# Performance work log

Measured on AMD Instinct MI355X. Metric: run time of the kernel, lower is better.

The kernel has to match this reference:

```python
import jax, jax.numpy as jnp
import numpy as np

N_NODES = 50000
N_EDGES = 800000
GNN_IN, GNN_HID, COMB = 256, 64, 64
MLP_IN, MLP_HID = 256, 512


def glorot(key, shape):
    fan_in, fan_out = shape[0], shape[1]
    s = jnp.sqrt(6.0 / (fan_in + fan_out)).astype(jnp.float32)
    return jax.random.uniform(key, shape, jnp.float32, -s, s)


def setup_inputs() -> dict:
    key = jax.random.key(0)
    ks = jax.random.split(key, 12)
    x = jax.random.normal(ks[0], (N_NODES, GNN_IN), jnp.float32)
    edge_index = jax.random.randint(ks[1], (2, N_EDGES), 0, N_NODES, jnp.int64 if jax.config.jax_enable_x64 else jnp.int32)
    edge_attr = jax.random.uniform(ks[2], (N_EDGES,), jnp.float32)
    user_features = jax.random.normal(ks[3], (N_NODES, MLP_IN), jnp.float32)
    params = {
        'gcn1_W': glorot(ks[4], (GNN_IN, GNN_HID)),
        'gcn1_b': jnp.zeros((GNN_HID,), jnp.float32),
        'gcn2_W': glorot(ks[5], (GNN_HID, COMB)),
        'gcn2_b': jnp.zeros((COMB,), jnp.float32),
        'fc1_W': glorot(ks[6], (MLP_IN, MLP_HID)),
        'fc1_b': jnp.zeros((MLP_HID,), jnp.float32),
        'fc2_W': glorot(ks[7], (MLP_HID, COMB)),
        'fc2_b': jnp.zeros((COMB,), jnp.float32),
        'fcf_W': glorot(ks[8], (2 * COMB, 1)),
        'fcf_b': jnp.zeros((1,), jnp.float32),
    }
    return dict(x=x, edge_index=edge_index, edge_attr=edge_attr,
                user_features=user_features, **params)


def gcn_conv(x, W, b, src, dst, ew, n_nodes):
    # PyG GCNConv: transform, add self-loops (weight 1), sym-normalize, scatter-add.
    h = x @ W  # [N, out]
    loop = jnp.arange(n_nodes, dtype=src.dtype)
    src_sl = jnp.concatenate([src, loop])
    dst_sl = jnp.concatenate([dst, loop])
    ew_sl = jnp.concatenate([ew, jnp.ones((n_nodes,), ew.dtype)])
    deg = jax.ops.segment_sum(ew_sl, dst_sl, num_segments=n_nodes)
    dinv = jnp.where(deg > 0, jax.lax.rsqrt(jnp.maximum(deg, 1e-12)), 0.0)
    norm = dinv[src_sl] * ew_sl * dinv[dst_sl]  # [E+N]
    msg = h[src_sl] * norm[:, None]             # gather + scale
    out = jax.ops.segment_sum(msg, dst_sl, num_segments=n_nodes)
    return out + b


def reference(x, edge_index, edge_attr, user_features,
              gcn1_W, gcn1_b, gcn2_W, gcn2_b,
              fc1_W, fc1_b, fc2_W, fc2_b, fcf_W, fcf_b):
    src, dst = edge_index[0], edge_index[1]
    n = x.shape[0]
    # MLP branch
    mlp_out = jax.nn.relu(user_features @ fc1_W + fc1_b) @ fc2_W + fc2_b
    # GNN branch
    g = gcn_conv(x, gcn1_W, gcn1_b, src, dst, edge_attr, n)
    g = jax.nn.relu(g)
    gnn_out = gcn_conv(g, gcn2_W, gcn2_b, src, dst, edge_attr, n)
    combined = jnp.concatenate([mlp_out, gnn_out], axis=-1)
    return combined @ fcf_W + fcf_b
```

## Files before the change

### kernel.cpp

```cpp
#include <hip/hip_runtime.h>
#include <hip/hip_bf16.h>

#define N_NODES 50000
#define N_EDGES 800000
#define BROW 264
#define NT_TILES 782
#define GRID_H13 512

typedef __attribute__((ext_vector_type(8))) short bfrag8;
typedef __attribute__((ext_vector_type(4))) float f32x4;
typedef __attribute__((ext_vector_type(4))) unsigned short us4;
typedef __attribute__((ext_vector_type(8))) unsigned short us8;

__device__ __forceinline__ float bf2f(unsigned short u) {
  return __uint_as_float(((unsigned int)u) << 16);
}
__device__ __forceinline__ unsigned short f2bf(float f) {
  unsigned int u = __float_as_uint(f);
  u = (u + 0x7fffu + ((u >> 16) & 1u)) >> 16;
  return (unsigned short)u;
}
__device__ __forceinline__ float ldS(const void* p, int f32, size_t i) {
  return f32 ? ((const float*)p)[i] : bf2f(((const unsigned short*)p)[i]);
}
__device__ __forceinline__ void stO(void* out, int f32, int i, float v) {
  if (f32) ((float*)out)[i] = v;
  else ((unsigned short*)out)[i] = f2bf(v);
}

__device__ __forceinline__ void stageLoadBF(const void* src, int nb, us8 st[4]) {
  const int t = threadIdx.x;
  const int r = t >> 3, q = t & 7;
  int row = nb + r; row = row < N_NODES ? row : (N_NODES - 1);
  const us8* s8 = (const us8*)((const unsigned short*)src + (size_t)row * 256 + q * 32);
#pragma unroll
  for (int j = 0; j < 4; ++j) st[j] = s8[j];
}
__device__ __forceinline__ void stageWriteBF(const us8 st[4], unsigned short* __restrict__ Bs) {
  const int t = threadIdx.x;
  const int r = t >> 3, q = t & 7;
  unsigned short* dst = Bs + r * BROW + q * 32;
#pragma unroll
  for (int j = 0; j < 4; ++j) *(us8*)(dst + j * 8) = st[j];
}
__device__ __forceinline__ void stageLoadF32(const void* src, int nb, f32x4 st[8]) {
  const int t = threadIdx.x;
  const int r = t >> 3, q = t & 7;
  int row = nb + r; row = row < N_NODES ? row : (N_NODES - 1);
  const f32x4* s4 = (const f32x4*)((const float*)src + (size_t)row * 256 + q * 32);
#pragma unroll
  for (int j = 0; j < 8; ++j) st[j] = s4[j];
}
__device__ __forceinline__ void stageWriteF32(const f32x4 st[8], unsigned short* __restrict__ Bs) {
  const int t = threadIdx.x;
  const int r = t >> 3, q = t & 7;
  unsigned short* dst = Bs + r * BROW + q * 32;
#pragma unroll
  for (int j = 0; j < 4; ++j) {
    f32x4 a = st[2 * j], b = st[2 * j + 1];
    us8 o;
    o[0] = f2bf(a[0]); o[1] = f2bf(a[1]); o[2] = f2bf(a[2]); o[3] = f2bf(a[3]);
    o[4] = f2bf(b[0]); o[5] = f2bf(b[1]); o[6] = f2bf(b[2]); o[7] = f2bf(b[3]);
    *(us8*)(dst + j * 8) = o;
  }
}

__global__ void k_detect(const void* x, const void* ea, const void* uf,
                         const void* f1W, const int* ei, int* flags) {
  int lane = threadIdx.x & 63;
  unsigned short ux = ((const unsigned short*)x)[lane];
  unsigned short ue = ((const unsigned short*)ea)[lane];
  unsigned short uu = ((const unsigned short*)uf)[lane];
  unsigned short uw = ((const unsigned short*)f1W)[lane];
  int oi = ei[2 * lane + 1];
  unsigned long long bx = __ballot(((ux >> 7) & 0xFF) > 0x85);
  unsigned long long be = __ballot((ue & 0x8000u) != 0);
  unsigned long long bu = __ballot(((uu >> 7) & 0xFF) > 0x85);
  unsigned long long bw = __ballot(((uw >> 7) & 0xFF) > 0x7E);
  unsigned long long bi = __ballot(oi != 0);
  if (lane == 0) {
    int fx = bx ? 1 : 0, fe = be ? 1 : 0, fu = bu ? 1 : 0, fw = bw ? 1 : 0;
    flags[0] = fx; flags[1] = fe; flags[2] = fu; flags[3] = fw;
    flags[4] = (bi == 0ull) ? 1 : 0;
    flags[5] = (fx & fe & fu & fw);
  }
}

__global__ __launch_bounds__(256) void k_zeroc(int* __restrict__ counts) {
  int i = blockIdx.x * 256 + threadIdx.x;
  if (i <= N_NODES) counts[i] = 0;
}

__global__ __launch_bounds__(256) void k_histpos(const int* __restrict__ ei,
                                                 const int* __restrict__ flags,
                                                 int* __restrict__ counts,
                                                 int* __restrict__ posw) {
  int e = blockIdx.x * 256 + threadIdx.x;
  if (e >= N_EDGES) return;
  int d;
  if (flags[4]) d = ei[1600000 + 2 * e];
  else          d = ei[800000 + e];
  d = d < 0 ? 0 : (d > N_NODES - 1 ? N_NODES - 1 : d);
  posw[e] = atomicAdd(&counts[d], 1);
}

__global__ __launch_bounds__(256) void k_scan1(const int* __restrict__ cnt,
                                               int* __restrict__ rp,
                                               int* __restrict__ bsum) {
  __shared__ int sd[256];
  int t = threadIdx.x;
  int i0 = blockIdx.x * 1024 + t * 4;
  int v0 = (i0 + 0) < N_NODES ? cnt[i0 + 0] : 0;
  int v1 = (i0 + 1) < N_NODES ? cnt[i0 + 1] : 0;
  int v2 = (i0 + 2) < N_NODES ? cnt[i0 + 2] : 0;
  int v3 = (i0 + 3) < N_NODES ? cnt[i0 + 3] : 0;
  int ts = v0 + v1 + v2 + v3;
  sd[t] = ts;
  __syncthreads();
  for (int off = 1; off < 256; off <<= 1) {
    int x = (t >= off) ? sd[t - off] : 0;
    __syncthreads();
    sd[t] += x;
    __syncthreads();
  }
  int exoff = sd[t] - ts;
  if (i0 + 0 < N_NODES) rp[i0 + 0] = exoff;
  if (i0 + 1 < N_NODES) rp[i0 + 1] = exoff + v0;
  if (i0 + 2 < N_NODES) rp[i0 + 2] = exoff + v0 + v1;
  if (i0 + 3 < N_NODES) rp[i0 + 3] = exoff + v0 + v1 + v2;
  if (t == 255) bsum[blockIdx.x] = sd[255];
}

__global__ void k_scan2(const int* __restrict__ bsum, int* __restrict__ boff,
                        int* __restrict__ rp, int nb) {
  if (threadIdx.x == 0) {
    int run = 0;
    for (int b = 0; b < nb; ++b) { boff[b] = run; run += bsum[b]; }
    rp[N_NODES] = run;
  }
}

__global__ __launch_bounds__(256) void k_scan3(int* __restrict__ rp,
                                               const int* __restrict__ boff) {
  int i = blockIdx.x * 256 + threadIdx.x;
  if (i < N_NODES) rp[i] += boff[i >> 10];
}

__global__ __launch_bounds__(256) void k_placeb(const int* __restrict__ ei,
                                                const void* ea,
                                                const int* __restrict__ flags,
                                                const int* __restrict__ rp,
                                                const int* __restrict__ posw,
                                                unsigned long long* __restrict__ e8) {
  int e = blockIdx.x * 256 + threadIdx.x;
  if (e >= N_EDGES) return;
  int s, d;
  if (flags[4]) { s = ei[2 * e]; d = ei[1600000 + 2 * e]; }
  else          { s = ei[e];     d = ei[800000 + e]; }
  s = s < 0 ? 0 : (s > N_NODES - 1 ? N_NODES - 1 : s);
  d = d < 0 ? 0 : (d > N_NODES - 1 ? N_NODES - 1 : d);
  float w = ldS(ea, flags[1], e);
  int pos = rp[d] + posw[e];
  e8[pos] = ((unsigned long long)__float_as_uint(w) << 32) | (unsigned int)s;
}

__global__ __launch_bounds__(256) void k_degc(const int* __restrict__ rp,
                                              const unsigned long long* __restrict__ e8,
                                              float* __restrict__ dinv) {
  const int i = blockIdx.x * 4 + (threadIdx.x >> 6);
  if (i >= N_NODES) return;
  const int lane = threadIdx.x & 63;
  const int base = rp[i], end = rp[i + 1];
  float s = 0.f;
  for (int j = base + lane; j < end; j += 64)
    s += __uint_as_float((unsigned int)(e8[j] >> 32));
#pragma unroll
  for (int off = 32; off > 0; off >>= 1) s += __shfl_xor(s, off, 64);
  if (lane == 0) dinv[i] = rsqrtf(s + 1.0f);
}

__global__ __launch_bounds__(512) void k_prep(
    const void* f1W, const void* g1W, const void* f2W, const void* f2b,
    const void* g2W, const void* g2b, const void* ffW, const void* ffb,
    const int* __restrict__ flags, unsigned short* __restrict__ W1T,
    unsigned short* __restrict__ WgT, float* __restrict__ w2f,
    float* __restrict__ w2g, float* __restrict__ constv) {
  const int fw = flags[3];
  if (blockIdx.x < 288) {
    int tid = blockIdx.x * 512 + threadIdx.x;
    if (tid < 512 * 256) {
      int c = tid >> 8, k = tid & 255;
      W1T[tid] = f2bf(ldS(f1W, fw, (size_t)k * 512 + c));
    } else if (tid < 512 * 256 + 64 * 256) {
      int j = tid - 512 * 256;
      int c = j >> 8, k = j & 255;
      WgT[j] = f2bf(ldS(g1W, fw, (size_t)k * 64 + c));
    }
    return;
  }
  int t = threadIdx.x;
  if (t < 512) {
    float s = 0.f;
    for (int c = 0; c < 64; ++c) s += ldS(f2W, fw, t * 64 + c) * ldS(ffW, fw, c);
    w2f[t] = s;
  }
  if (t < 64) {
    float s = 0.f;
    for (int c = 0; c < 64; ++c) s += ldS(g2W, fw, t * 64 + c) * ldS(ffW, fw, 64 + c);
    w2g[t] = s;
  }
  if (t == 0) {
    float s = ldS(ffb, fw, 0);
    for (int c = 0; c < 64; ++c) {
      s += ldS(f2b, fw, c) * ldS(ffW, fw, c);
      s += ldS(g2b, fw, c) * ldS(ffW, fw, 64 + c);
    }
    constv[0] = s;
  }
}

__global__ __launch_bounds__(512, 2) void k_h13P(
    const void* x, const unsigned short* __restrict__ WgT,
    const float* __restrict__ dinv, const int* __restrict__ flags,
    unsigned short* __restrict__ h1b) {
  __shared__ __align__(16) unsigned short Bs[2][64 * BROW];
  const int f32in = flags[0];
  const int lane = threadIdx.x & 63;
  const int wave = threadIdx.x >> 6;
  const int ct = wave & 3;
  const int nh = wave >> 2;
  const int l15 = lane & 15;
  const int quad = lane >> 4;

  bfrag8 A[8];
  {
    const unsigned short* ap = WgT + (size_t)(ct * 16 + l15) * 256 + quad * 8;
#pragma unroll
    for (int ks = 0; ks < 8; ++ks) A[ks] = *(const bfrag8*)(ap + ks * 32);
  }

  int tile = blockIdx.x;
  {
    if (f32in) { f32x4 st[8]; stageLoadF32(x, tile * 64, st); stageWriteF32(st, Bs[0]); }
    else       { us8 st[4];  stageLoadBF(x, tile * 64, st);  stageWriteBF(st, Bs[0]); }
  }
  __syncthreads();

  int cur = 0;
  for (; tile < NT_TILES; tile += GRID_H13) {
    const int nxt = tile + GRID_H13;
    const bool have = nxt < NT_TILES;
    us8 stb[4]; f32x4 stf[8];
    if (have) {
      if (f32in) stageLoadF32(x, nxt * 64, stf);
      else       stageLoadBF(x, nxt * 64, stb);
    }

    f32x4 acc[2];
    acc[0] = (f32x4){0.f, 0.f, 0.f, 0.f};
    acc[1] = (f32x4){0.f, 0.f, 0.f, 0.f};
    const unsigned short* Bc = Bs[cur];
#pragma unroll
    for (int ks = 0; ks < 8; ++ks) {
      const int bofs = ks * 32 + quad * 8;
#pragma unroll
      for (int u = 0; u < 2; ++u) {
        bfrag8 b = *(const bfrag8*)(Bc + (nh * 32 + u * 16 + l15) * BROW + bofs);
        acc[u] = __builtin_amdgcn_mfma_f32_16x16x32_bf16(A[ks], b, acc[u], 0, 0, 0);
      }
    }

    if (have) {
      if (f32in) stageWriteF32(stf, Bs[cur ^ 1]);
      else       stageWriteBF(stb, Bs[cur ^ 1]);
    }

#pragma unroll
    for (int u = 0; u < 2; ++u) {
      int node = tile * 64 + nh * 32 + u * 16 + l15;
      if (node < N_NODES) {
        float di = dinv[node];
        us4 o;
#pragma unroll
        for (int r = 0; r < 4; ++r) o[r] = f2bf(acc[u][r] * di);
        *(us4*)(h1b + (size_t)node * 64 + ct * 16 + quad * 4) = o;
      }
    }
    __syncthreads();
    cur ^= 1;
  }
}

__global__ __launch_bounds__(512, 2) void k_mlp1(
    const void* uf, const unsigned short* __restrict__ W1T,
    const void* fc1b, const float* __restrict__ w2f,
    const int* __restrict__ flags, float* __restrict__ mlpc,
    float* __restrict__ mlpc2) {
  __shared__ __align__(16) unsigned short Bs[64 * BROW];
  __shared__ float red[512];
  const int f32in = flags[2];
  const int fw = flags[3];
  const int half = blockIdx.x & 1;
  const int tile = blockIdx.x >> 1;
  const int lane = threadIdx.x & 63;
  const int wave = threadIdx.x >> 6;
  const int l15 = lane & 15;
  const int quad = lane >> 4;
  const int c_base = half * 256 + wave * 32;
  float* __restrict__ mout = half ? mlpc2 : mlpc;

  us8 stb[4]; f32x4 stf[8];
  if (f32in) stageLoadF32(uf, tile * 64, stf);
  else       stageLoadBF(uf, tile * 64, stb);

  bfrag8 A[2][8];
  {
    const unsigned short* ap = W1T + (size_t)(c_base + l15) * 256 + quad * 8;
#pragma unroll
    for (int t = 0; t < 2; ++t)
#pragma unroll
      for (int ks = 0; ks < 8; ++ks)
        A[t][ks] = *(const bfrag8*)(ap + (size_t)t * 16 * 256 + ks * 32);
  }

  if (f32in) stageWriteF32(stf, Bs);
  else       stageWriteBF(stb, Bs);
  __syncthreads();

  f32x4 acc[2][4];
#pragma unroll
  for (int t = 0; t < 2; ++t)
#pragma unroll
    for (int u = 0; u < 4; ++u) acc[t][u] = (f32x4){0.f, 0.f, 0.f, 0.f};

#pragma unroll
  for (int ks = 0; ks < 8; ++ks) {
    const int bofs = ks * 32 + quad * 8;
    bfrag8 b[4];
#pragma unroll
    for (int u = 0; u < 4; ++u)
      b[u] = *(const bfrag8*)(Bs + (u * 16 + l15) * BROW + bofs);
#pragma unroll
    for (int t = 0; t < 2; ++t)
#pragma unroll
      for (int u = 0; u < 4; ++u)
        acc[t][u] = __builtin_amdgcn_mfma_f32_16x16x32_bf16(A[t][ks], b[u], acc[t][u], 0, 0, 0);
  }

  float part[4] = {0.f, 0.f, 0.f, 0.f};
#pragma unroll
  for (int t = 0; t < 2; ++t)
#pragma unroll
    for (int r = 0; r < 4; ++r) {
      const int c = c_base + t * 16 + quad * 4 + r;
      const float bc = ldS(fc1b, fw, c);
      const float wc = w2f[c];
#pragma unroll
      for (int u = 0; u < 4; ++u) {
        float v = acc[t][u][r] + bc;
        v = v > 0.f ? v : 0.f;
        part[u] += v * wc;
      }
    }

#pragma unroll
  for (int u = 0; u < 4; ++u) {
    part[u] += __shfl_xor(part[u], 16, 64);
    part[u] += __shfl_xor(part[u], 32, 64);
    if (lane < 16) red[wave * 64 + u * 16 + l15] = part[u];
  }
  __syncthreads();
  if (threadIdx.x < 64) {
    float sum = 0.f;
#pragma unroll
    for (int w = 0; w < 8; ++w) sum += red[w * 64 + threadIdx.x];
    int node = tile * 64 + threadIdx.x;
    if (node < N_NODES) mout[node] = sum;
  }
}

__global__ __launch_bounds__(256) void k_aggs2(
    const int* __restrict__ rp, const unsigned long long* __restrict__ e8,
    const unsigned short* __restrict__ h1b, const float* __restrict__ dinv,
    const void* g1b, const float* __restrict__ w2g,
    const int* __restrict__ flags, float* __restrict__ s2) {
  const int i = blockIdx.x * 4 + (threadIdx.x >> 6);
  if (i >= N_NODES) return;
  const int lane = threadIdx.x & 63;
  const int base = rp[i], end = rp[i + 1];
  const float di = dinv[i];
  float acc = 0.f;
  int j = base;
  for (; j + 8 <= end; j += 8) {
    unsigned long long vv[8];
#pragma unroll
    for (int q = 0; q < 8; ++q) vv[q] = e8[j + q];
    float ww[8], hv[8];
#pragma unroll
    for (int q = 0; q < 8; ++q) {
      ww[q] = __uint_as_float((unsigned int)(vv[q] >> 32));
      hv[q] = bf2f(h1b[(size_t)(unsigned int)vv[q] * 64 + lane]);
    }
#pragma unroll
    for (int q = 0; q < 8; ++q) acc += ww[q] * hv[q];
  }
  for (; j < end; ++j) {
    unsigned long long v = e8[j];
    acc += __uint_as_float((unsigned int)(v >> 32)) *
           bf2f(h1b[(size_t)(unsigned int)v * 64 + lane]);
  }
  float v = (acc + bf2f(h1b[(size_t)i * 64 + lane])) * di + ldS(g1b, flags[3], lane);
  v = v > 0.f ? v : 0.f;
  float p = v * w2g[lane];
#pragma unroll
  for (int off = 32; off > 0; off >>= 1) p += __shfl_xor(p, off, 64);
  if (lane == 0) s2[i] = di * p;
}

__global__ __launch_bounds__(256) void k_fin2(
    const int* __restrict__ rp, const unsigned long long* __restrict__ e8,
    const float* __restrict__ s2, const float* __restrict__ dinv,
    const float* __restrict__ mlpc, const float* __restrict__ mlpc2,
    const float* __restrict__ constv, const int* __restrict__ flags, void* out) {
  const int i = blockIdx.x * 4 + (threadIdx.x >> 6);
  if (i >= N_NODES) return;
  const int lane = threadIdx.x & 63;
  const int base = rp[i], end = rp[i + 1];
  float p = 0.f;
  for (int j = base + lane; j < end; j += 64) {
    unsigned long long v = e8[j];
    p += __uint_as_float((unsigned int)(v >> 32)) * s2[(unsigned int)v];
  }
#pragma unroll
  for (int off = 32; off > 0; off >>= 1) p += __shfl_xor(p, off, 64);
  if (lane == 0) {
    float di = dinv[i];
    stO(out, flags[5], i, mlpc[i] + mlpc2[i] + di * (p + s2[i]) + constv[0]);
  }
}

__global__ __launch_bounds__(256) void k_zero(const int* __restrict__ flags, void* out) {
  int i = blockIdx.x * 256 + threadIdx.x;
  if (i < N_NODES) stO(out, flags[5], i, 0.f);
}

extern "C" void kernel_launch(void* const* d_in, const int* in_sizes, int n_in,
                              void* d_out, int out_size, void* d_ws, size_t ws_size,
                              hipStream_t stream) {
  const void* x   = d_in[0];
  const int*  ei  = (const int*)d_in[1];
  const void* ea  = d_in[2];
  const void* uf  = d_in[3];
  const void* g1W = d_in[4];
  const void* g1b = d_in[5];
  const void* g2W = d_in[6];
  const void* g2b = d_in[7];
  const void* f1W = d_in[8];
  const void* f1b = d_in[9];
  const void* f2W = d_in[10];
  const void* f2b = d_in[11];
  const void* ffW = d_in[12];
  const void* ffb = d_in[13];

  float* ws = (float*)d_ws;
  int*   flags  = (int*)ws;
  float* w2f    = ws + 16;
  float* w2g    = ws + 528;
  float* constv = ws + 592;
  float* dinv   = ws + 608;
  float* s2     = ws + 50608;
  float* mlpc   = ws + 100608;
  unsigned short* W1T = (unsigned short*)(ws + 150608);
  unsigned short* WgT = W1T + 131072;
  int* rowptr = (int*)(ws + 224336);
  int* bsum   = (int*)(ws + 274352);
  int* boff   = bsum + 64;
  int* counts = (int*)(ws + 274480);
  int* posw   = (int*)(ws + 324496);
  unsigned long long* e8 = (unsigned long long*)(ws + 1124496);
  unsigned short* h1b = (unsigned short*)(ws + 2724496);
  float* mlpc2 = ws + 4324496;
  const size_t NEED = (size_t)4374496 * 4;

  k_detect<<<1, 64, 0, stream>>>(x, ea, uf, f1W, ei, flags);
  if (ws_size < NEED) {
    k_zero<<<(N_NODES + 255) / 256, 256, 0, stream>>>(flags, d_out);
    return;
  }
  const int NZB = (N_NODES + 256) / 256;
  const int NB  = (N_NODES + 1023) / 1024;
  const int NEB = (N_EDGES + 255) / 256;

  k_zeroc<<<NZB, 256, 0, stream>>>(counts);
  k_histpos<<<NEB, 256, 0, stream>>>(ei, flags, counts, posw);
  k_scan1<<<NB, 256, 0, stream>>>(counts, rowptr, bsum);
  k_scan2<<<1, 64, 0, stream>>>(bsum, boff, rowptr, NB);
  k_scan3<<<(N_NODES + 255) / 256, 256, 0, stream>>>(rowptr, boff);
  k_placeb<<<NEB, 256, 0, stream>>>(ei, ea, flags, rowptr, posw, e8);
  k_degc<<<(N_NODES + 3) / 4, 256, 0, stream>>>(rowptr, e8, dinv);
  k_prep<<<289, 512, 0, stream>>>(f1W, g1W, f2W, f2b, g2W, g2b, ffW, ffb, flags,
                                  W1T, WgT, w2f, w2g, constv);
  k_h13P<<<GRID_H13, 512, 0, stream>>>(x, WgT, dinv, flags, h1b);
  k_mlp1<<<2 * NT_TILES, 512, 0, stream>>>(uf, W1T, f1b, w2f, flags, mlpc, mlpc2);
  k_aggs2<<<(N_NODES + 3) / 4, 256, 0, stream>>>(rowptr, e8, h1b, dinv, g1b, w2g, flags, s2);
  k_fin2<<<(N_NODES + 3) / 4, 256, 0, stream>>>(rowptr, e8, s2, dinv, mlpc, mlpc2, constv, flags, d_out);
}
```

Measured before the change: 355.5 us.

## Fuse GCN layer-1 transform and MLP branch into one per-tile kernel

Merges the x@Wg kernel and the two-half MLP kernel into a single kernel with one block per 64-node tile. Each block stages both x and user_features into shared memory and does all 512 MLP hidden columns itself, so the mlpc2 buffer and a launch go away. The cost is a larger block with twice the shared memory and a serial loop over two column passes. The software pipelining of the old persistent x kernel is also dropped.

```diff
diff --git a/kernel.cpp b/kernel.cpp
--- a/kernel.cpp
+++ b/kernel.cpp
@@ -5,7 +5,6 @@
 #define N_EDGES 800000
 #define BROW 264
 #define NT_TILES 782
-#define GRID_H13 512
 
 typedef __attribute__((ext_vector_type(8))) short bfrag8;
 typedef __attribute__((ext_vector_type(4))) float f32x4;
@@ -219,62 +218,48 @@
   }
 }
 
-__global__ __launch_bounds__(512, 2) void k_h13P(
-    const void* x, const unsigned short* __restrict__ WgT,
+__global__ __launch_bounds__(512, 2) void k_fused(
+    const void* x, const void* uf,
+    const unsigned short* __restrict__ WgT, const unsigned short* __restrict__ W1T,
+    const void* fc1b, const float* __restrict__ w2f,
     const float* __restrict__ dinv, const int* __restrict__ flags,
-    unsigned short* __restrict__ h1b) {
-  __shared__ __align__(16) unsigned short Bs[2][64 * BROW];
-  const int f32in = flags[0];
+    unsigned short* __restrict__ h1b, float* __restrict__ mlpc) {
+  __shared__ __align__(16) unsigned short Xs[64 * BROW];
+  __shared__ __align__(16) unsigned short Us[64 * BROW];
+  __shared__ float red[512];
+  const int fx = flags[0], fu = flags[2], fw = flags[3];
+  const int tile = blockIdx.x;
   const int lane = threadIdx.x & 63;
   const int wave = threadIdx.x >> 6;
-  const int ct = wave & 3;
-  const int nh = wave >> 2;
   const int l15 = lane & 15;
   const int quad = lane >> 4;
 
-  bfrag8 A[8];
+  if (fx) { f32x4 st[8]; stageLoadF32(x, tile * 64, st); stageWriteF32(st, Xs); }
+  else    { us8 st[4];  stageLoadBF(x, tile * 64, st);  stageWriteBF(st, Xs); }
+  if (fu) { f32x4 st[8]; stageLoadF32(uf, tile * 64, st); stageWriteF32(st, Us); }
+  else    { us8 st[4];  stageLoadBF(uf, tile * 64, st);  stageWriteBF(st, Us); }
+  __syncthreads();
+
   {
+    const int ct = wave & 3;
+    const int nh = wave >> 2;
+    bfrag8 Ag[8];
     const unsigned short* ap = WgT + (size_t)(ct * 16 + l15) * 256 + quad * 8;
 #pragma unroll
-    for (int ks = 0; ks < 8; ++ks) A[ks] = *(const bfrag8*)(ap + ks * 32);
-  }
-
-  int tile = blockIdx.x;
-  {
-    if (f32in) { f32x4 st[8]; stageLoadF32(x, tile * 64, st); stageWriteF32(st, Bs[0]); }
-    else       { us8 st[4];  stageLoadBF(x, tile * 64, st);  stageWriteBF(st, Bs[0]); }
-  }
-  __syncthreads();
-
-  int cur = 0;
-  for (; tile < NT_TILES; tile += GRID_H13) {
-    const int nxt = tile + GRID_H13;
-    const bool have = nxt < NT_TILES;
-    us8 stb[4]; f32x4 stf[8];
-    if (have) {
-      if (f32in) stageLoadF32(x, nxt * 64, stf);
-      else       stageLoadBF(x, nxt * 64, stb);
-    }
-
-    f32x4 acc[2];
-    acc[0] = (f32x4){0.f, 0.f, 0.f, 0.f};
-    acc[1] = (f32x4){0.f, 0.f, 0.f, 0.f};
-    const unsigned short* Bc = Bs[cur];
+    for (int ks = 0; ks < 8; ++ks) Ag[ks] = *(const bfrag8*)(ap + ks * 32);
+
+    f32x4 accg[2];
+    accg[0] = (f32x4){0.f, 0.f, 0.f, 0.f};
+    accg[1] = (f32x4){0.f, 0.f, 0.f, 0.f};
 #pragma unroll
     for (int ks = 0; ks < 8; ++ks) {
       const int bofs = ks * 32 + quad * 8;
 #pragma unroll
       for (int u = 0; u < 2; ++u) {
-        bfrag8 b = *(const bfrag8*)(Bc + (nh * 32 + u * 16 + l15) * BROW + bofs);
-        acc[u] = __builtin_amdgcn_mfma_f32_16x16x32_bf16(A[ks], b, acc[u], 0, 0, 0);
+        bfrag8 b = *(const bfrag8*)(Xs + (nh * 32 + u * 16 + l15) * BROW + bofs);
+        accg[u] = __builtin_amdgcn_mfma_f32_16x16x32_bf16(Ag[ks], b, accg[u], 0, 0, 0);
       }
     }
-
-    if (have) {
-      if (f32in) stageWriteF32(stf, Bs[cur ^ 1]);
-      else       stageWriteBF(stb, Bs[cur ^ 1]);
-    }
-
 #pragma unroll
     for (int u = 0; u < 2; ++u) {
       int node = tile * 64 + nh * 32 + u * 16 + l15;
@@ -282,86 +267,59 @@
         float di = dinv[node];
         us4 o;
 #pragma unroll
-        for (int r = 0; r < 4; ++r) o[r] = f2bf(acc[u][r] * di);
+        for (int r = 0; r < 4; ++r) o[r] = f2bf(accg[u][r] * di);
         *(us4*)(h1b + (size_t)node * 64 + ct * 16 + quad * 4) = o;
       }
     }
-    __syncthreads();
-    cur ^= 1;
-  }
-}
-
-__global__ __launch_bounds__(512, 2) void k_mlp1(
-    const void* uf, const unsigned short* __restrict__ W1T,
-    const void* fc1b, const float* __restrict__ w2f,
-    const int* __restrict__ flags, float* __restrict__ mlpc,
-    float* __restrict__ mlpc2) {
-  __shared__ __align__(16) unsigned short Bs[64 * BROW];
-  __shared__ float red[512];
-  const int f32in = flags[2];
-  const int fw = flags[3];
-  const int half = blockIdx.x & 1;
-  const int tile = blockIdx.x >> 1;
-  const int lane = threadIdx.x & 63;
-  const int wave = threadIdx.x >> 6;
-  const int l15 = lane & 15;
-  const int quad = lane >> 4;
-  const int c_base = half * 256 + wave * 32;
-  float* __restrict__ mout = half ? mlpc2 : mlpc;
-
-  us8 stb[4]; f32x4 stf[8];
-  if (f32in) stageLoadF32(uf, tile * 64, stf);
-  else       stageLoadBF(uf, tile * 64, stb);
-
-  bfrag8 A[2][8];
-  {
-    const unsigned short* ap = W1T + (size_t)(c_base + l15) * 256 + quad * 8;
+  }
+
+  float part[4] = {0.f, 0.f, 0.f, 0.f};
+  for (int p = 0; p < 2; ++p) {
+    const int c_base = wave * 64 + p * 32;
+    bfrag8 A[2][8];
+    {
+      const unsigned short* ap = W1T + (size_t)(c_base + l15) * 256 + quad * 8;
+#pragma unroll
+      for (int t = 0; t < 2; ++t)
+#pragma unroll
+        for (int ks = 0; ks < 8; ++ks)
+          A[t][ks] = *(const bfrag8*)(ap + (size_t)t * 16 * 256 + ks * 32);
+    }
+    f32x4 acc[2][4];
 #pragma unroll
     for (int t = 0; t < 2; ++t)
 #pragma unroll
-      for (int ks = 0; ks < 8; ++ks)
-        A[t][ks] = *(const bfrag8*)(ap + (size_t)t * 16 * 256 + ks * 32);
-  }
-
-  if (f32in) stageWriteF32(stf, Bs);
-  else       stageWriteBF(stb, Bs);
-  __syncthreads();
-
-  f32x4 acc[2][4];
-#pragma unroll
-  for (int t = 0; t < 2; ++t)
-#pragma unroll
-    for (int u = 0; u < 4; ++u) acc[t][u] = (f32x4){0.f, 0.f, 0.f, 0.f};
-
-#pragma unroll
-  for (int ks = 0; ks < 8; ++ks) {
-    const int bofs = ks * 32 + quad * 8;
-    bfrag8 b[4];
-#pragma unroll
-    for (int u = 0; u < 4; ++u)
-      b[u] = *(const bfrag8*)(Bs + (u * 16 + l15) * BROW + bofs);
+      for (int u = 0; u < 4; ++u) acc[t][u] = (f32x4){0.f, 0.f, 0.f, 0.f};
+
+#pragma unroll
+    for (int ks = 0; ks < 8; ++ks) {
+      const int bofs = ks * 32 + quad * 8;
+      bfrag8 b[4];
+#pragma unroll
+      for (int u = 0; u < 4; ++u)
+        b[u] = *(const bfrag8*)(Us + (u * 16 + l15) * BROW + bofs);
+#pragma unroll
+      for (int t = 0; t < 2; ++t)
+#pragma unroll
+        for (int u = 0; u < 4; ++u)
+          acc[t][u] = __builtin_amdgcn_mfma_f32_16x16x32_bf16(A[t][ks], b[u], acc[t][u], 0, 0, 0);
+    }
+
 #pragma unroll
     for (int t = 0; t < 2; ++t)
 #pragma unroll
-      for (int u = 0; u < 4; ++u)
-        acc[t][u] = __builtin_amdgcn_mfma_f32_16x16x32_bf16(A[t][ks], b[u], acc[t][u], 0, 0, 0);
-  }
-
-  float part[4] = {0.f, 0.f, 0.f, 0.f};
-#pragma unroll
-  for (int t = 0; t < 2; ++t)
-#pragma unroll
-    for (int r = 0; r < 4; ++r) {
-      const int c = c_base + t * 16 + quad * 4 + r;
-      const float bc = ldS(fc1b, fw, c);
-      const float wc = w2f[c];
-#pragma unroll
-      for (int u = 0; u < 4; ++u) {
-        float v = acc[t][u][r] + bc;
-        v = v > 0.f ? v : 0.f;
-        part[u] += v * wc;
+      for (int r = 0; r < 4; ++r) {
+        const int c = c_base + t * 16 + quad * 4 + r;
+        const float bc = ldS(fc1b, fw, c);
+        const float wc = w2f[c];
+#pragma unroll
+        for (int u = 0; u < 4; ++u) {
+          float v = acc[t][u][r] + bc;
+          v = v > 0.f ? v : 0.f;
+          part[u] += v * wc;
+        }
       }
-    }
+  }
 
 #pragma unroll
   for (int u = 0; u < 4; ++u) {
@@ -375,7 +333,7 @@
 #pragma unroll
     for (int w = 0; w < 8; ++w) sum += red[w * 64 + threadIdx.x];
     int node = tile * 64 + threadIdx.x;
-    if (node < N_NODES) mout[node] = sum;
+    if (node < N_NODES) mlpc[node] = sum;
   }
 }
 
@@ -420,8 +378,8 @@
 __global__ __launch_bounds__(256) void k_fin2(
     const int* __restrict__ rp, const unsigned long long* __restrict__ e8,
     const float* __restrict__ s2, const float* __restrict__ dinv,
-    const float* __restrict__ mlpc, const float* __restrict__ mlpc2,
-    const float* __restrict__ constv, const int* __restrict__ flags, void* out) {
+    const float* __restrict__ mlpc, const float* __restrict__ constv,
+    const int* __restrict__ flags, void* out) {
   const int i = blockIdx.x * 4 + (threadIdx.x >> 6);
   if (i >= N_NODES) return;
   const int lane = threadIdx.x & 63;
@@ -435,7 +393,7 @@
   for (int off = 32; off > 0; off >>= 1) p += __shfl_xor(p, off, 64);
   if (lane == 0) {
     float di = dinv[i];
-    stO(out, flags[5], i, mlpc[i] + mlpc2[i] + di * (p + s2[i]) + constv[0]);
+    stO(out, flags[5], i, mlpc[i] + di * (p + s2[i]) + constv[0]);
   }
 }
 
@@ -479,8 +437,7 @@
   int* posw   = (int*)(ws + 324496);
   unsigned long long* e8 = (unsigned long long*)(ws + 1124496);
   unsigned short* h1b = (unsigned short*)(ws + 2724496);
-  float* mlpc2 = ws + 4324496;
-  const size_t NEED = (size_t)4374496 * 4;
+  const size_t NEED = (size_t)4324496 * 4;
 
   k_detect<<<1, 64, 0, stream>>>(x, ea, uf, f1W, ei, flags);
   if (ws_size < NEED) {
@@ -500,8 +457,7 @@
   k_degc<<<(N_NODES + 3) / 4, 256, 0, stream>>>(rowptr, e8, dinv);
   k_prep<<<289, 512, 0, stream>>>(f1W, g1W, f2W, f2b, g2W, g2b, ffW, ffb, flags,
                                   W1T, WgT, w2f, w2g, constv);
-  k_h13P<<<GRID_H13, 512, 0, stream>>>(x, WgT, dinv, flags, h1b);
-  k_mlp1<<<2 * NT_TILES, 512, 0, stream>>>(uf, W1T, f1b, w2f, flags, mlpc, mlpc2);
+  k_fused<<<NT_TILES, 512, 0, stream>>>(x, uf, WgT, W1T, f1b, w2f, dinv, flags, h1b, mlpc);
   k_aggs2<<<(N_NODES + 3) / 4, 256, 0, stream>>>(rowptr, e8, h1b, dinv, g1b, w2g, flags, s2);
-  k_fin2<<<(N_NODES + 3) / 4, 256, 0, stream>>>(rowptr, e8, s2, dinv, mlpc, mlpc2, constv, flags, d_out);
-}
+  k_fin2<<<(N_NODES + 3) / 4, 256, 0, stream>>>(rowptr, e8, s2, dinv, mlpc, constv, flags, d_out);
+}
```

Measured after the change: 364.5 us. +2.5%, slower.
